# Kernel optimization log

Measured on AMD Instinct MI355X. Metric: run time of the kernel, lower is better.

Reference implementation:

```python
import jax, jax.numpy as jnp
import numpy as np
import math

# B queries, N complex ambient dim, M codebook entries, S payload dim, K quad nodes
B, N, M, S, K = 1024, 128, 8192, 256, 8
EPS_TOTAL = 1e-3
OVERLAP, ANISO = 0.25, 0.75
_t, _w = np.polynomial.hermite.hermgauss(K)
GH_T = jnp.asarray(_t, jnp.float32)
GH_W = jnp.asarray(_w, jnp.float32)


def _init_sigmas():
    # mirrors CPSFFusedCodebook._init_sigmas (log-space for numerical safety at N=128)
    rho = 1.0 + ANISO
    logV = (N / 2.0) * math.log(math.pi) - math.lgamma(N / 2.0 + 1.0)
    log_r = (math.log(OVERLAP) - math.log(M) - logV - math.log(rho)) / N
    r_perp = math.exp(log_r)
    s_perp = 2.0 * math.pi * r_perp ** 2
    return rho * rho * s_perp, s_perp


def setup_inputs() -> dict:
    key = jax.random.key(0)
    ks = jax.random.split(key, 12)
    u = lambda k, sh: jax.random.uniform(k, sh, jnp.float32, -1.0, 1.0)
    s_par, s_perp = _init_sigmas()
    return {
        "z_re": u(ks[0], (B, N)), "z_im": u(ks[1], (B, N)),
        "d_re": u(ks[2], (B, N)), "d_im": u(ks[3], (B, N)),
        "zj_re": 0.5 * u(ks[4], (M, N)), "zj_im": 0.5 * u(ks[5], (M, N)),
        "dj_re": 0.5 * u(ks[6], (M, N)), "dj_im": 0.5 * u(ks[7], (M, N)),
        "T_re": u(ks[8], (M, S)), "T_im": u(ks[9], (M, S)),
        "alpha": jax.random.uniform(ks[10], (M,), jnp.float32, 0.5, 1.5),
        "sigma_par": jnp.full((M,), s_par, jnp.float32),
        "sigma_perp": jnp.full((M,), s_perp, jnp.float32),
    }


def _unit(xr, xi):
    n = jnp.sqrt(jnp.sum(xr * xr + xi * xi, -1, keepdims=True))
    n = jnp.where(n == 0, jnp.ones_like(n), n)
    return xr / n, xi / n


def _forward(z_re, z_im, d_re, d_im, zj_re, zj_im, dj_re, dj_im,
             T_re, T_im, alpha, sigma_par, sigma_perp):
    tiny = jnp.float32(np.finfo(np.float32).tiny)
    dur, dui = _unit(d_re, d_im)          # autonorm_vec_d
    djr, dji = _unit(dj_re, dj_im)        # autonorm_vec_d_j
    a = jnp.maximum(alpha, tiny)
    sp = jnp.maximum(sigma_par, tiny)
    sq = jnp.maximum(sigma_perp, tiny)

    # proj[b,m] = <d_j, z - z_j> (conj-linear in d_j); all via GEMMs, no [B,M,N] tensor
    pr = z_re @ djr.T + z_im @ dji.T - jnp.sum(djr * zj_re + dji * zj_im, -1)[None, :]
    pi = z_im @ djr.T - z_re @ dji.T - jnp.sum(djr * zj_im - dji * zj_re, -1)[None, :]

    # |z - z_j|^2 via GEMM expansion
    dz2 = (jnp.sum(z_re * z_re + z_im * z_im, -1)[:, None]
           + jnp.sum(zj_re * zj_re + zj_im * zj_im, -1)[None, :]
           - 2.0 * (z_re @ zj_re.T + z_im @ zj_im.T))
    perp2 = jnp.maximum(dz2 - (pr * pr + pi * pi), 0.0)  # component orthogonal to d_j

    # Gauss-Hermite quadrature along the codebook direction, scaled per-code
    scale = jnp.sqrt(sp / jnp.pi)                     # [M]
    t = GH_T[None, :] * scale[:, None]                # [M,K] quad offsets
    par2 = (pr[:, :, None] - t[None]) ** 2 + (pi * pi)[:, :, None]   # [B,M,K]
    env = jnp.exp(-jnp.pi * (par2 / sp[None, :, None]
                             + (perp2 / sq[None, :])[:, :, None]))
    rho = jnp.einsum('bmk,k->bm', env, GH_W) * (scale / jnp.sqrt(jnp.pi))[None, :]

    # angular alignment |<d_j, d>|^2
    ar = dur @ djr.T + dui @ dji.T
    ai = dui @ djr.T - dur @ dji.T
    align = ar * ar + ai * ai

    w = a[None, :] * align * rho                      # [B,M] real mixture weights
    den = jnp.sum(w, -1) + EPS_TOTAL                  # [B]
    out_re = (w @ T_re) / den[:, None]                # [B,S]
    out_im = (w @ T_im) / den[:, None]
    return jnp.stack([out_re, out_im], -1)            # [B,S,2] == complex [B,S]


def reference(z_re, z_im, d_re, d_im, zj_re, zj_im, dj_re, dj_im,
              T_re, T_im, alpha, sigma_par, sigma_perp):
    return _forward(z_re, z_im, d_re, d_im, zj_re, zj_im, dj_re, dj_im,
                    T_re, T_im, alpha, sigma_par, sigma_perp)
```

## Files before the change

kernel.cpp:

```cpp
#include <hip/hip_runtime.h>
#include <math.h>

#define Bq 1024
#define Nn 128
#define Mm 8192
#define Ss 256

typedef _Float16 f16;
typedef _Float16 f16x8 __attribute__((ext_vector_type(8)));
typedef _Float16 f16x4 __attribute__((ext_vector_type(4)));
typedef float f32x4 __attribute__((ext_vector_type(4)));

#define PI_F 3.14159265358979323846f
#define INV_SQRT_PI 0.5641895835477563f
#define TINY_F 1.17549435e-38f
#define EPS_TOTAL 1e-3f
#define WSC 1024.0f

#define GLOAD16(g, l) \
    __builtin_amdgcn_global_load_lds((const __attribute__((address_space(1))) void*)(g), \
                                     (__attribute__((address_space(3))) void*)(l), 16, 0, 0)

__global__ void cpsf_prep_pack(
    const float* __restrict__ z_re, const float* __restrict__ z_im,
    const float* __restrict__ d_re, const float* __restrict__ d_im,
    const float* __restrict__ zj_re, const float* __restrict__ zj_im,
    const float* __restrict__ dj_re, const float* __restrict__ dj_im,
    const float* __restrict__ T_re, const float* __restrict__ T_im,
    const float* __restrict__ alpha, const float* __restrict__ sp_,
    const float* __restrict__ sq_, float* __restrict__ z2,
    float* __restrict__ cm, f16* __restrict__ Az, f16* __restrict__ Bp,
    f16* __restrict__ Tt, int Mc, int m0g, int n0, int n1, int n2, int mshift)
{
    __shared__ float tsm[2 * 64 * 65];
    const int bx = blockIdx.x;
    const int tid = threadIdx.x;
    const int wid = tid >> 6;
    const int l = tid & 63;

    if (bx < n0) {
        const int b = bx * 4 + wid;
        const int o = b * Nn;
        float dr0 = d_re[o + l], dr1 = d_re[o + l + 64];
        float di0 = d_im[o + l], di1 = d_im[o + l + 64];
        float zr0 = z_re[o + l], zr1 = z_re[o + l + 64];
        float zi0 = z_im[o + l], zi1 = z_im[o + l + 64];
        float sd = dr0*dr0 + di0*di0 + dr1*dr1 + di1*di1;
        float sz = zr0*zr0 + zi0*zi0 + zr1*zr1 + zi1*zi1;
#pragma unroll
        for (int off = 1; off < 64; off <<= 1) {
            sd += __shfl_xor(sd, off);
            sz += __shfl_xor(sz, off);
        }
        float nd = sqrtf(sd);
        nd = (nd == 0.0f) ? 1.0f : nd;
        float inv = 1.0f / nd;
        if (l == 0) z2[b] = sz;
        int map = l >> 5, c = l & 31;
        int k8 = (c & 15) * 8;
        const float* src = (map == 0) ? ((c < 16) ? z_re : z_im)
                                      : ((c < 16) ? d_re : d_im);
        float s = (map == 0) ? 1.0f : inv;
        float4 v0 = *(const float4*)(src + (size_t)b * Nn + k8);
        float4 v1 = *(const float4*)(src + (size_t)b * Nn + k8 + 4);
        f16x8 ov = {(f16)(v0.x*s), (f16)(v0.y*s), (f16)(v0.z*s), (f16)(v0.w*s),
                    (f16)(v1.x*s), (f16)(v1.y*s), (f16)(v1.z*s), (f16)(v1.w*s)};
        *(f16x8*)(Az + ((size_t)l * 1024 + b) * 8) = ov;
    } else if (bx < n0 + n1) {
        const int m = (bx - n0) * 4 + wid;
        const int o = m * Nn;
        float dr0 = dj_re[o + l], dr1 = dj_re[o + l + 64];
        float di0 = dj_im[o + l], di1 = dj_im[o + l + 64];
        float zr0 = zj_re[o + l], zr1 = zj_re[o + l + 64];
        float zi0 = zj_im[o + l], zi1 = zj_im[o + l + 64];
        float snd = dr0*dr0 + di0*di0 + dr1*dr1 + di1*di1;
        float sc1 = dr0*zr0 + di0*zi0 + dr1*zr1 + di1*zi1;
        float sc2 = dr0*zi0 - di0*zr0 + dr1*zi1 - di1*zr1;
        float sz2 = zr0*zr0 + zi0*zi0 + zr1*zr1 + zi1*zi1;
#pragma unroll
        for (int off = 1; off < 64; off <<= 1) {
            snd += __shfl_xor(snd, off);
            sc1 += __shfl_xor(sc1, off);
            sc2 += __shfl_xor(sc2, off);
            sz2 += __shfl_xor(sz2, off);
        }
        if (l == 0) {
            float nd = sqrtf(snd);
            nd = (nd == 0.0f) ? 1.0f : nd;
            float inv = 1.0f / nd;
            cm[0*Mm + m] = inv;
            cm[1*Mm + m] = sc1 * inv;
            cm[2*Mm + m] = sc2 * inv;
            cm[3*Mm + m] = sz2;
            float sp = fmaxf(sp_[m], TINY_F);
            float sq = fmaxf(sq_[m], TINY_F);
            float sc = sqrtf(sp / PI_F);
            cm[4*Mm + m] = PI_F / sp;
            cm[5*Mm + m] = PI_F / sq;
            cm[6*Mm + m] = fmaxf(alpha[m], TINY_F) * sc * INV_SQRT_PI;
            cm[7*Mm + m] = sc;
        }
    } else if (bx < n0 + n1 + n2) {
        int idx = (bx - n0 - n1) * 256 + tid;
        int m = idx & (Mc - 1);
        int pc = idx >> mshift;
        int p = pc >> 5, c = pc & 31;
        int mg = m0g + m;
        int hi = (c >= 16);
        int k8 = (c & 15) * 8;
        const float* src;
        float sgn = 1.0f;
        if (p == 0)      src = hi ? dj_im : dj_re;
        else if (p == 1) { src = hi ? dj_re : dj_im; sgn = hi ? 1.0f : -1.0f; }
        else             src = hi ? zj_im : zj_re;
        float4 v0 = *(const float4*)(src + (size_t)mg * Nn + k8);
        float4 v1 = *(const float4*)(src + (size_t)mg * Nn + k8 + 4);
        f16x8 o = {(f16)(v0.x*sgn), (f16)(v0.y*sgn), (f16)(v0.z*sgn), (f16)(v0.w*sgn),
                   (f16)(v1.x*sgn), (f16)(v1.y*sgn), (f16)(v1.z*sgn), (f16)(v1.w*sgn)};
        *(f16x8*)(Bp + (size_t)idx * 8) = o;
    } else {
        const int bt = bx - n0 - n1 - n2;
        const int nmb = Mc >> 6;
        const int mb = (bt & (nmb - 1)) * 64, sb = (bt / nmb) * 64;
        float* tr = tsm;
        float* ti = tsm + 64 * 65;
        const int i0 = tid >> 6, jj0 = tid & 63;
#pragma unroll
        for (int it = 0; it < 16; ++it) {
            int i = it * 4 + i0;
            tr[i * 65 + jj0] = T_re[(size_t)(m0g + mb + i) * Ss + sb + jj0];
            ti[i * 65 + jj0] = T_im[(size_t)(m0g + mb + i) * Ss + sb + jj0];
        }
        __syncthreads();
#pragma unroll
        for (int it = 0; it < 16; ++it) {
            int jj = it * 4 + i0;
            int sp = (sb + jj) * 2;
            Tt[(size_t)sp * Mc + mb + jj0]       = (f16)tr[jj0 * 65 + jj];
            Tt[(size_t)(sp + 1) * Mc + mb + jj0] = (f16)ti[jj0 * 65 + jj];
        }
    }
}

__global__ __launch_bounds__(256, 3) void cpsf_gemm_w(
    const f16* __restrict__ Az, const f16* __restrict__ Bp,
    const float* __restrict__ cm, const float* __restrict__ z2v,
    f16* __restrict__ wbuf, float* __restrict__ den, int Mc, int m0g)
{
    __shared__ __align__(16) f16 sm[2 * 1280 * 8];
    const int tid = threadIdx.x;
    const int wid = tid >> 6;
    const int lane = tid & 63;
    const int q = lane >> 4;
    const int li = lane & 15;

    const int nmt = gridDim.x;
    const int sbid = blockIdx.x + nmt * blockIdx.y;
    const int xcd = sbid & 7;
    const int jb = sbid >> 3;
    const int mpg = nmt >> 3;
    const int mtile = xcd * mpg + (jb & (mpg - 1));
    const int btile = jb / mpg;
    const int mb0 = mtile * 64;
    const int bb0 = btile * 64;
    const int wb0 = (wid >> 1) * 32;
    const int wm0 = (wid & 1) * 32;
    const int BUFO = 1280 * 8;

    const f16* gp[5];
    size_t gstep[5];
    f16* lb[5];
#pragma unroll
    for (int i = 0; i < 5; ++i) {
        const f16* src;
        size_t st;
        if (i == 0) {
            src = Az + ((size_t)wid * 1024 + bb0 + lane) * 8;
            st = (size_t)4 * 1024 * 8;
        } else if (i == 1) {
            src = Az + ((size_t)(32 + wid) * 1024 + bb0 + lane) * 8;
            st = (size_t)4 * 1024 * 8;
        } else {
            int j = (i - 2) * 4 + wid;
            int g = j / 3, p = j % 3;
            src = Bp + ((size_t)(p * 32 + g) * Mc + mb0 + lane) * 8;
            st = (size_t)4 * Mc * 8;
        }
        gp[i] = src; gstep[i] = st;
        lb[i] = sm + (size_t)(i * 256 + wid * 64) * 8;
    }

    f32x4 accP[2][2][3];
    f32x4 accQ[2][2][2];
#pragma unroll
    for (int t = 0; t < 2; ++t)
#pragma unroll
        for (int u = 0; u < 2; ++u) {
#pragma unroll
            for (int p = 0; p < 3; ++p) accP[t][u][p] = (f32x4){0.f,0.f,0.f,0.f};
#pragma unroll
            for (int p = 0; p < 2; ++p) accQ[t][u][p] = (f32x4){0.f,0.f,0.f,0.f};
        }

#pragma unroll
    for (int i = 0; i < 5; ++i) { GLOAD16(gp[i], lb[i]); gp[i] += gstep[i]; }

#pragma unroll
    for (int ks = 0; ks < 8; ++ks) {
        const int p = ks & 1;
        if (ks > 0) {
            __builtin_amdgcn_sched_barrier(0);
            __builtin_amdgcn_s_barrier();
        }
        if (ks < 7) {
#pragma unroll
            for (int i = 0; i < 5; ++i) { GLOAD16(gp[i], lb[i] + (p ^ 1) * BUFO); gp[i] += gstep[i]; }
            asm volatile("s_waitcnt vmcnt(5)" ::: "memory");
        } else {
            asm volatile("s_waitcnt vmcnt(0)" ::: "memory");
        }
        __builtin_amdgcn_sched_barrier(0);
        __builtin_amdgcn_s_barrier();

        const f16* bs = sm + p * BUFO;
        f16x8 az[2], au[2], bf[3][2];
#pragma unroll
        for (int t = 0; t < 2; ++t) {
            az[t] = *(const f16x8*)(bs + (size_t)(q * 64 + wb0 + t * 16 + li) * 8);
            au[t] = *(const f16x8*)(bs + (size_t)(256 + q * 64 + wb0 + t * 16 + li) * 8);
        }
#pragma unroll
        for (int pp = 0; pp < 3; ++pp)
#pragma unroll
            for (int u = 0; u < 2; ++u)
                bf[pp][u] = *(const f16x8*)(bs + (size_t)(512 + q * 192 + pp * 64 + wm0 + u * 16 + li) * 8);

        __builtin_amdgcn_s_setprio(1);
#pragma unroll
        for (int t = 0; t < 2; ++t)
#pragma unroll
            for (int u = 0; u < 2; ++u) {
#pragma unroll
                for (int pp = 0; pp < 3; ++pp)
                    accP[t][u][pp] = __builtin_amdgcn_mfma_f32_16x16x32_f16(az[t], bf[pp][u], accP[t][u][pp], 0, 0, 0);
#pragma unroll
                for (int pp = 0; pp < 2; ++pp)
                    accQ[t][u][pp] = __builtin_amdgcn_mfma_f32_16x16x32_f16(au[t], bf[pp][u], accQ[t][u][pp], 0, 0, 0);
            }
        __builtin_amdgcn_s_setprio(0);
    }

    const float GT[8] = {-2.9306374202572440f, -1.9816567566958429f,
                         -1.1571937124467802f, -0.3811869902073221f,
                          0.3811869902073221f,  1.1571937124467802f,
                          1.9816567566958429f,  2.9306374202572440f};
    const float GW[8] = {1.9960407221136762e-04f, 1.7077983007413475e-02f,
                         2.0780232581489188e-01f, 6.6114701255824129e-01f,
                         6.6114701255824129e-01f, 2.0780232581489188e-01f,
                         1.7077983007413475e-02f, 1.9960407221136762e-04f};

    float iv[2], c1[2], c2[2], zj2[2], isp[2], isq[2], cf[2], scl[2];
#pragma unroll
    for (int u = 0; u < 2; ++u) {
        int mg = m0g + mb0 + wm0 + u * 16 + li;
        iv[u]  = cm[0*Mm + mg];
        c1[u]  = cm[1*Mm + mg];  c2[u]  = cm[2*Mm + mg];
        zj2[u] = cm[3*Mm + mg];  isp[u] = cm[4*Mm + mg];
        isq[u] = cm[5*Mm + mg];  cf[u]  = cm[6*Mm + mg];
        scl[u] = cm[7*Mm + mg];
    }

    float dsum[2][4];
#pragma unroll
    for (int t = 0; t < 2; ++t)
#pragma unroll
        for (int r = 0; r < 4; ++r) dsum[t][r] = 0.f;

#pragma unroll
    for (int t = 0; t < 2; ++t) {
#pragma unroll
        for (int r = 0; r < 4; ++r) {
            const int b = bb0 + wb0 + t * 16 + q * 4 + r;
            const float z2b = z2v[b];
#pragma unroll
            for (int u = 0; u < 2; ++u) {
                float pr = accP[t][u][0][r] * iv[u] - c1[u];
                float pi = accP[t][u][1][r] * iv[u] - c2[u];
                float dz2 = z2b + zj2[u] - 2.0f * accP[t][u][2][r];
                float perp2 = fmaxf(dz2 - pr * pr - pi * pi, 0.0f);
                float base = -(isq[u] * perp2 + isp[u] * pi * pi);
                float rho = 0.0f;
#pragma unroll
                for (int k = 0; k < 8; ++k) {
                    float dd = pr - scl[u] * GT[k];
                    rho = fmaf(GW[k], __expf(base - isp[u] * dd * dd), rho);
                }
                float ar = accQ[t][u][0][r] * iv[u], ai = accQ[t][u][1][r] * iv[u];
                float wv = cf[u] * (ar * ar + ai * ai) * rho;
                dsum[t][r] += wv;
                wbuf[(size_t)b * Mc + mb0 + wm0 + u * 16 + li] = (f16)(wv * WSC);
            }
        }
    }
#pragma unroll
    for (int t = 0; t < 2; ++t)
#pragma unroll
        for (int r = 0; r < 4; ++r) {
            float v = dsum[t][r];
            v += __shfl_xor(v, 1);
            v += __shfl_xor(v, 2);
            v += __shfl_xor(v, 4);
            v += __shfl_xor(v, 8);
            if (li == 0) atomicAdd(den + bb0 + wb0 + t * 16 + q * 4 + r, v);
        }
}

__global__ __launch_bounds__(256, 2) void cpsf_gemm_out(
    const f16* __restrict__ wbuf, const f16* __restrict__ Tt,
    float* __restrict__ osl, int Mc, int Kw, int zs)
{
    __shared__ __align__(16) f16 sm[2 * 2048 * 8];
    const int tid = threadIdx.x;
    const int wid = tid >> 6;
    const int lane = tid & 63;
    const int q = lane >> 4;
    const int li = lane & 15;

    const int bid = blockIdx.x;
    const int xcd = bid & 7;
    const int j = bid >> 3;
    const int s = j / zs;
    const int g = xcd * zs + (j % zs);
    const int zb = g >> 3;
    const int yb = g & 7;
    const int sb0 = s * 128;
    const int bb0 = yb * 128;
    const int kz0 = zb * Kw;
    float* oz = osl + (size_t)zb * ((size_t)Bq * 512);
    const int wb0 = (wid >> 1) * 64;
    const int ws0 = (wid & 1) * 64;
    const int BUFO = 2048 * 8;

    const f16* gp[8];
    f16* lb[8];
#pragma unroll
    for (int i = 0; i < 8; ++i) {
        int c = i * 4 + wid;
        const f16* src;
        if (c < 16) {
            int gch = c >> 1, row = (c & 1) * 64 + lane;
            src = wbuf + (size_t)(bb0 + row) * Mc + kz0 + gch * 8;
        } else {
            int c2 = c - 16;
            int gch = c2 >> 1, row = (c2 & 1) * 64 + lane;
            src = Tt + (size_t)(sb0 + row) * Mc + kz0 + gch * 8;
        }
        gp[i] = src;
        lb[i] = sm + (size_t)(c * 64) * 8;
    }

    f32x4 acc[4][4];
#pragma unroll
    for (int t = 0; t < 4; ++t)
#pragma unroll
        for (int u = 0; u < 4; ++u) acc[t][u] = (f32x4){0.f,0.f,0.f,0.f};

#pragma unroll
    for (int i = 0; i < 8; ++i) { GLOAD16(gp[i], lb[i]); gp[i] += 64; }

    const int nk = Kw >> 6;
    for (int kc = 0; kc < nk; ++kc) {
        const int p = kc & 1;
        if (kc > 0) {
            __builtin_amdgcn_sched_barrier(0);
            __builtin_amdgcn_s_barrier();
        }
        if (kc + 1 < nk) {
#pragma unroll
            for (int i = 0; i < 8; ++i) { GLOAD16(gp[i], lb[i] + (p ^ 1) * BUFO); gp[i] += 64; }
            asm volatile("s_waitcnt vmcnt(8)" ::: "memory");
        } else {
            asm volatile("s_waitcnt vmcnt(0)" ::: "memory");
        }
        __builtin_amdgcn_sched_barrier(0);
        __builtin_amdgcn_s_barrier();

        const f16* bs = sm + p * BUFO;
#pragma unroll
        for (int kk = 0; kk < 2; ++kk) {
            f16x8 af[4], bf[4];
#pragma unroll
            for (int t = 0; t < 4; ++t)
                af[t] = *(const f16x8*)(bs + (size_t)((kk * 4 + q) * 128 + wb0 + t * 16 + li) * 8);
#pragma unroll
            for (int u = 0; u < 4; ++u)
                bf[u] = *(const f16x8*)(bs + (size_t)(1024 + (kk * 4 + q) * 128 + ws0 + u * 16 + li) * 8);
            __builtin_amdgcn_s_setprio(1);
#pragma unroll
            for (int t = 0; t < 4; ++t)
#pragma unroll
                for (int u = 0; u < 4; ++u)
                    acc[t][u] = __builtin_amdgcn_mfma_f32_16x16x32_f16(af[t], bf[u], acc[t][u], 0, 0, 0);
            __builtin_amdgcn_s_setprio(0);
        }
    }
#pragma unroll
    for (int t = 0; t < 4; ++t)
#pragma unroll
        for (int u = 0; u < 4; ++u)
#pragma unroll
            for (int r = 0; r < 4; ++r)
                oz[(size_t)(bb0 + wb0 + t * 16 + q * 4 + r) * 512 + sb0 + ws0 + u * 16 + li] =
                    acc[t][u][r];
}

__global__ void cpsf_fin(const float* __restrict__ osl, const float* __restrict__ den,
                         float* __restrict__ out, int Z)
{
    int i = (blockIdx.x * 256 + threadIdx.x) * 4;
    float4 s = {0.f, 0.f, 0.f, 0.f};
    for (int z = 0; z < Z; ++z) {
        float4 v = *(const float4*)(osl + (size_t)z * ((size_t)Bq * 512) + i);
        s.x += v.x; s.y += v.y; s.z += v.z; s.w += v.w;
    }
    float d = 1.0f / ((den[i >> 9] + EPS_TOTAL) * WSC);
    float4 o = {s.x * d, s.y * d, s.z * d, s.w * d};
    *(float4*)(out + i) = o;
}

extern "C" void kernel_launch(void* const* d_in, const int* in_sizes, int n_in,
                              void* d_out, int out_size, void* d_ws, size_t ws_size,
                              hipStream_t stream)
{
    (void)in_sizes; (void)n_in; (void)out_size;
    const float* z_re  = (const float*)d_in[0];
    const float* z_im  = (const float*)d_in[1];
    const float* d_re  = (const float*)d_in[2];
    const float* d_im  = (const float*)d_in[3];
    const float* zj_re = (const float*)d_in[4];
    const float* zj_im = (const float*)d_in[5];
    const float* dj_re = (const float*)d_in[6];
    const float* dj_im = (const float*)d_in[7];
    const float* T_re  = (const float*)d_in[8];
    const float* T_im  = (const float*)d_in[9];
    const float* alpha = (const float*)d_in[10];
    const float* s_par = (const float*)d_in[11];
    const float* s_perp= (const float*)d_in[12];

    const size_t SL = (size_t)Bq * 512 * 4;
    const size_t fixedA = 4096 + 4096 + (size_t)8 * Mm * 4 + (size_t)Bq * 512 * 2;

    int Mc = 0, Z = 0;
    const int Zopt[3] = {16, 8, 4};
    const int Mopt[4] = {8192, 4096, 2048, 1024};
    for (int zi = 0; zi < 3 && !Mc; ++zi)
        for (int mi = 0; mi < 4; ++mi) {
            int Zc = Zopt[zi], Mcc = Mopt[mi];
            int nch = Mm / Mcc;
            if (Zc % nch) continue;
            if (Mcc / (Zc / nch) < 64) continue;
            size_t need = (size_t)Zc * SL + fixedA + (size_t)4608 * Mcc;
            if (need <= ws_size) { Mc = Mcc; Z = Zc; break; }
        }
    if (!Mc) { Mc = 1024; Z = 8; }
    const int nch = Mm / Mc;
    const int zs = Z / nch;
    const int Kw = Mc / zs;
    const int mshift = 31 - __builtin_clz((unsigned)Mc);

    char* w8 = (char*)d_ws;
    const size_t o_sl  = 0;
    const size_t o_den = o_sl + (size_t)Z * SL;
    const size_t o_z2  = o_den + 4096;
    const size_t o_cm  = o_z2 + 4096;
    const size_t o_az  = o_cm + (size_t)8 * Mm * 4;
    const size_t o_ch  = o_az + (size_t)Bq * 512 * 2;

    float* osl = (float*)(w8 + o_sl);
    float* den = (float*)(w8 + o_den);
    float* z2  = (float*)(w8 + o_z2);
    float* cm  = (float*)(w8 + o_cm);
    f16*   Az  = (f16*)(w8 + o_az);
    f16*   Bp  = (f16*)(w8 + o_ch);
    f16*   Tt  = (f16*)(w8 + o_ch + (size_t)1536 * Mc);
    f16*   wb  = (f16*)(w8 + o_ch + (size_t)2560 * Mc);

    hipMemsetAsync(w8 + o_den, 0, 4096, stream);

    for (int ci = 0; ci < nch; ++ci) {
        const int m0 = ci * Mc;
        const int n0 = (ci == 0) ? 256 : 0;
        const int n1 = (ci == 0) ? Mm / 4 : 0;
        const int n2 = (96 * Mc) / 256;
        const int n3 = (Mc / 64) * (Ss / 64);
        cpsf_prep_pack<<<n0 + n1 + n2 + n3, 256, 0, stream>>>(
            z_re, z_im, d_re, d_im, zj_re, zj_im, dj_re, dj_im, T_re, T_im,
            alpha, s_par, s_perp, z2, cm, Az, Bp, Tt, Mc, m0, n0, n1, n2, mshift);
        cpsf_gemm_w<<<dim3(Mc / 64, Bq / 64), 256, 0, stream>>>(
            Az, Bp, cm, z2, wb, den, Mc, m0);
        cpsf_gemm_out<<<32 * zs, 256, 0, stream>>>(
            wb, Tt, osl + (size_t)ci * zs * ((size_t)Bq * 512), Mc, Kw, zs);
    }
    cpsf_fin<<<(Bq * 512) / 1024, 256, 0, stream>>>(osl, den, (float*)d_out, Z);
}
```

Measured before the change: 218.5 us.

## Shrink output GEMM tiles to 64x64, cut split-K to 8, raise occupancy

The output GEMM moves from 128x128 tiles per block to 64x64 tiles, so each wave computes a 32x32 sub-tile and LDS use is halved. Split-K drops from 16 to 8 slices, giving more K work per block and fewer partial-sum slabs for the final reduction to read. Launch bounds on both GEMM kernels rise to 4 blocks per CU. Smaller tiles lower data reuse per loaded byte and may add register pressure in the weight GEMM, in exchange for more blocks in flight and less reduction traffic.

```diff
diff --git a/kernel.cpp b/kernel.cpp
--- a/kernel.cpp
+++ b/kernel.cpp
@@ -142,7 +142,7 @@
     }
 }
 
-__global__ __launch_bounds__(256, 3) void cpsf_gemm_w(
+__global__ __launch_bounds__(256, 4) void cpsf_gemm_w(
     const f16* __restrict__ Az, const f16* __restrict__ Bp,
     const float* __restrict__ cm, const float* __restrict__ z2v,
     f16* __restrict__ wbuf, float* __restrict__ den, int Mc, int m0g)
@@ -315,58 +315,54 @@
         }
 }
 
-__global__ __launch_bounds__(256, 2) void cpsf_gemm_out(
+__global__ __launch_bounds__(256, 4) void cpsf_gemm_out(
     const f16* __restrict__ wbuf, const f16* __restrict__ Tt,
-    float* __restrict__ osl, int Mc, int Kw, int zs)
+    float* __restrict__ osl, int Mc, int Kw)
 {
-    __shared__ __align__(16) f16 sm[2 * 2048 * 8];
+    __shared__ __align__(16) f16 sm[2 * 1024 * 8];
     const int tid = threadIdx.x;
     const int wid = tid >> 6;
     const int lane = tid & 63;
     const int q = lane >> 4;
     const int li = lane & 15;
 
-    const int bid = blockIdx.x;
-    const int xcd = bid & 7;
-    const int j = bid >> 3;
-    const int s = j / zs;
-    const int g = xcd * zs + (j % zs);
-    const int zb = g >> 3;
-    const int yb = g & 7;
-    const int sb0 = s * 128;
-    const int bb0 = yb * 128;
+    const int nblk = gridDim.x;
+    const int cpx = nblk >> 3;
+    const int lin = (blockIdx.x & 7) * cpx + (blockIdx.x >> 3);
+    const int zb = lin >> 7;
+    const int r7 = lin & 127;
+    const int bt = r7 >> 3, st = r7 & 7;
+    const int bb0 = bt * 64;
+    const int sb0 = st * 64;
     const int kz0 = zb * Kw;
     float* oz = osl + (size_t)zb * ((size_t)Bq * 512);
-    const int wb0 = (wid >> 1) * 64;
-    const int ws0 = (wid & 1) * 64;
-    const int BUFO = 2048 * 8;
-
-    const f16* gp[8];
-    f16* lb[8];
-#pragma unroll
-    for (int i = 0; i < 8; ++i) {
+    const int wb0 = (wid >> 1) * 32;
+    const int ws0 = (wid & 1) * 32;
+    const int BUFO = 1024 * 8;
+
+    const f16* gp[4];
+    f16* lb[4];
+#pragma unroll
+    for (int i = 0; i < 4; ++i) {
         int c = i * 4 + wid;
         const f16* src;
-        if (c < 16) {
-            int gch = c >> 1, row = (c & 1) * 64 + lane;
-            src = wbuf + (size_t)(bb0 + row) * Mc + kz0 + gch * 8;
+        if (c < 8) {
+            src = wbuf + (size_t)(bb0 + lane) * Mc + kz0 + c * 8;
         } else {
-            int c2 = c - 16;
-            int gch = c2 >> 1, row = (c2 & 1) * 64 + lane;
-            src = Tt + (size_t)(sb0 + row) * Mc + kz0 + gch * 8;
+            src = Tt + (size_t)(sb0 + lane) * Mc + kz0 + (c - 8) * 8;
         }
         gp[i] = src;
         lb[i] = sm + (size_t)(c * 64) * 8;
     }
 
-    f32x4 acc[4][4];
-#pragma unroll
-    for (int t = 0; t < 4; ++t)
-#pragma unroll
-        for (int u = 0; u < 4; ++u) acc[t][u] = (f32x4){0.f,0.f,0.f,0.f};
-
-#pragma unroll
-    for (int i = 0; i < 8; ++i) { GLOAD16(gp[i], lb[i]); gp[i] += 64; }
+    f32x4 acc[2][2];
+#pragma unroll
+    for (int t = 0; t < 2; ++t)
+#pragma unroll
+        for (int u = 0; u < 2; ++u) acc[t][u] = (f32x4){0.f,0.f,0.f,0.f};
+
+#pragma unroll
+    for (int i = 0; i < 4; ++i) { GLOAD16(gp[i], lb[i]); gp[i] += 64; }
 
     const int nk = Kw >> 6;
     for (int kc = 0; kc < nk; ++kc) {
@@ -377,8 +373,8 @@
         }
         if (kc + 1 < nk) {
 #pragma unroll
-            for (int i = 0; i < 8; ++i) { GLOAD16(gp[i], lb[i] + (p ^ 1) * BUFO); gp[i] += 64; }
-            asm volatile("s_waitcnt vmcnt(8)" ::: "memory");
+            for (int i = 0; i < 4; ++i) { GLOAD16(gp[i], lb[i] + (p ^ 1) * BUFO); gp[i] += 64; }
+            asm volatile("s_waitcnt vmcnt(4)" ::: "memory");
         } else {
             asm volatile("s_waitcnt vmcnt(0)" ::: "memory");
         }
@@ -388,26 +384,27 @@
         const f16* bs = sm + p * BUFO;
 #pragma unroll
         for (int kk = 0; kk < 2; ++kk) {
-            f16x8 af[4], bf[4];
-#pragma unroll
-            for (int t = 0; t < 4; ++t)
-                af[t] = *(const f16x8*)(bs + (size_t)((kk * 4 + q) * 128 + wb0 + t * 16 + li) * 8);
-#pragma unroll
-            for (int u = 0; u < 4; ++u)
-                bf[u] = *(const f16x8*)(bs + (size_t)(1024 + (kk * 4 + q) * 128 + ws0 + u * 16 + li) * 8);
+            const int g = kk * 4 + q;
+            f16x8 af[2], bf[2];
+#pragma unroll
+            for (int t = 0; t < 2; ++t)
+                af[t] = *(const f16x8*)(bs + (size_t)(g * 64 + wb0 + t * 16 + li) * 8);
+#pragma unroll
+            for (int u = 0; u < 2; ++u)
+                bf[u] = *(const f16x8*)(bs + (size_t)(512 + g * 64 + ws0 + u * 16 + li) * 8);
             __builtin_amdgcn_s_setprio(1);
 #pragma unroll
-            for (int t = 0; t < 4; ++t)
-#pragma unroll
-                for (int u = 0; u < 4; ++u)
+            for (int t = 0; t < 2; ++t)
+#pragma unroll
+                for (int u = 0; u < 2; ++u)
                     acc[t][u] = __builtin_amdgcn_mfma_f32_16x16x32_f16(af[t], bf[u], acc[t][u], 0, 0, 0);
             __builtin_amdgcn_s_setprio(0);
         }
     }
 #pragma unroll
-    for (int t = 0; t < 4; ++t)
-#pragma unroll
-        for (int u = 0; u < 4; ++u)
+    for (int t = 0; t < 2; ++t)
+#pragma unroll
+        for (int u = 0; u < 2; ++u)
 #pragma unroll
             for (int r = 0; r < 4; ++r)
                 oz[(size_t)(bb0 + wb0 + t * 16 + q * 4 + r) * 512 + sb0 + ws0 + u * 16 + li] =
@@ -451,14 +448,15 @@
     const size_t fixedA = 4096 + 4096 + (size_t)8 * Mm * 4 + (size_t)Bq * 512 * 2;
 
     int Mc = 0, Z = 0;
-    const int Zopt[3] = {16, 8, 4};
+    const int Zopt[2] = {8, 4};
     const int Mopt[4] = {8192, 4096, 2048, 1024};
-    for (int zi = 0; zi < 3 && !Mc; ++zi)
+    for (int zi = 0; zi < 2 && !Mc; ++zi)
         for (int mi = 0; mi < 4; ++mi) {
             int Zc = Zopt[zi], Mcc = Mopt[mi];
             int nch = Mm / Mcc;
             if (Zc % nch) continue;
-            if (Mcc / (Zc / nch) < 64) continue;
+            int Kwc = Mcc / (Zc / nch);
+            if (Kwc < 64 || (Kwc & 63)) continue;
             size_t need = (size_t)Zc * SL + fixedA + (size_t)4608 * Mcc;
             if (need <= ws_size) { Mc = Mcc; Z = Zc; break; }
         }
@@ -498,8 +496,8 @@
             alpha, s_par, s_perp, z2, cm, Az, Bp, Tt, Mc, m0, n0, n1, n2, mshift);
         cpsf_gemm_w<<<dim3(Mc / 64, Bq / 64), 256, 0, stream>>>(
             Az, Bp, cm, z2, wb, den, Mc, m0);
-        cpsf_gemm_out<<<32 * zs, 256, 0, stream>>>(
-            wb, Tt, osl + (size_t)ci * zs * ((size_t)Bq * 512), Mc, Kw, zs);
+        cpsf_gemm_out<<<128 * zs, 256, 0, stream>>>(
+            wb, Tt, osl + (size_t)ci * zs * ((size_t)Bq * 512), Mc, Kw);
     }
     cpsf_fin<<<(Bq * 512) / 1024, 256, 0, stream>>>(osl, den, (float*)d_out, Z);
 }
```

Measured after the change: 244.5 us. +11.9%, slower.
